# Kernel optimization log

Hardware: AMD Instinct MI355X
Metric: run time of the kernel (lower is better)

Reference implementation:

```python
import jax, jax.numpy as jnp
import numpy as np

B, H, S, DK = 2, 16, 2048, 64


def setup_inputs() -> dict:
    key = jax.random.key(0)
    kq, kk, kv, km = jax.random.split(key, 4)
    query = jax.random.normal(kq, (B, H, S, DK), dtype=jnp.float32)
    key_t = jax.random.normal(kk, (B, H, S, DK), dtype=jnp.float32)
    value = jax.random.normal(kv, (B, H, S, DK), dtype=jnp.float32)
    mask = jax.random.randint(km, (1, 1, S, S), 0, 2, dtype=jnp.int32)
    return {"query": query, "key": key_t, "value": value, "mask": mask}


def reference(query, key, value, mask):
    # scores: [B, H, Sq, Sk]
    d_k = query.shape[-1]
    scale = 1.0 / jnp.sqrt(jnp.asarray(d_k, dtype=query.dtype))
    scores = jnp.einsum("bhqd,bhkd->bhqk", query, key) * scale
    scores = jnp.where(mask == 0, jnp.asarray(-1e9, dtype=scores.dtype), scores)
    attention_weights = jax.nn.softmax(scores, axis=-1)
    # dropout is identity in eval mode (deterministic reference)
    output = jnp.einsum("bhqk,bhkd->bhqd", attention_weights, value)
    return output, attention_weights
```

## Files before the change

kernel.cpp:

```cpp
#include <hip/hip_runtime.h>
#include <hip/hip_bf16.h>


namespace {

constexpr int Bc = 2, Hc = 16, Sc = 2048, Dc = 64;
constexpr int QT = 64;
constexpr int KT = 64;
constexpr int NKV = Sc / KT;
constexpr int NQB = Sc / QT;
constexpr int NBH = Bc * Hc;
constexpr float SCALE2 = 0.125f * 1.44269504088896340736f;

constexpr int PS_OFF = 0;
constexpr int KS_OFF = 8192;
constexpr int VS_OFF = 24576;

constexpr size_t BITS_BYTES = (size_t)Sc * Sc / 8;
constexpr size_t IMG_BYTES  = (size_t)NBH * NKV * 8192;
constexpr size_t KIMG_OFF   = BITS_BYTES;
constexpr size_t VIMG_OFF   = BITS_BYTES + IMG_BYTES;
constexpr size_t WS_FULL    = BITS_BYTES + 2 * IMG_BYTES;

using short8 = __attribute__((ext_vector_type(8))) short;
using f32x4  = __attribute__((ext_vector_type(4))) float;
using u32x4  = __attribute__((ext_vector_type(4))) unsigned;

__device__ __forceinline__ int swz(int row, int bytecol) {
    return row * 128 + (bytecol ^ ((row & 7) << 4));
}

__device__ __forceinline__ unsigned cvtpk(float a, float b) {
    unsigned r;
    asm("v_cvt_pk_bf16_f32 %0, %1, %2" : "=v"(r) : "v"(a), "v"(b));
    return r;
}

__device__ __forceinline__ f32x4 mfma16(short8 a, short8 b, f32x4 c) {
    return __builtin_amdgcn_mfma_f32_16x16x32_bf16(a, b, c, 0, 0, 0);
}
__device__ __forceinline__ short8 ldlds(const char* lds, int off, int row,
                                        int bytecol) {
    return *reinterpret_cast<const short8*>(lds + off + swz(row, bytecol));
}

__device__ __forceinline__ void bar_lgkm() {
    __builtin_amdgcn_sched_barrier(0);
    asm volatile("s_waitcnt lgkmcnt(0)" ::: "memory");
    __builtin_amdgcn_s_barrier();
    __builtin_amdgcn_sched_barrier(0);
}
__device__ __forceinline__ void fence_lgkm() {
    __builtin_amdgcn_sched_barrier(0);
    asm volatile("s_waitcnt lgkmcnt(0)" ::: "memory");
    __builtin_amdgcn_sched_barrier(0);
}

__device__ __forceinline__ void ldk_g(const float* __restrict__ src, int tid,
                                      float4 reg[4]) {
    #pragma unroll
    for (int i = 0; i < 4; ++i) {
        int ch = tid + 256 * i;
        int r = ch >> 4, d0 = (ch & 15) << 2;
        reg[i] = *reinterpret_cast<const float4*>(src + (size_t)r * Dc + d0);
    }
}
__device__ __forceinline__ void stk_g(char* dst, int off, int tid,
                                      const float4 reg[4]) {
    #pragma unroll
    for (int i = 0; i < 4; ++i) {
        int ch = tid + 256 * i;
        int r = ch >> 4, d0 = (ch & 15) << 2;
        uint2 pk; pk.x = cvtpk(reg[i].x, reg[i].y);
        pk.y = cvtpk(reg[i].z, reg[i].w);
        *reinterpret_cast<uint2*>(dst + off + swz(r, d0 * 2)) = pk;
    }
}
__device__ __forceinline__ void ldv_g(const float* __restrict__ src, int tid,
                                      float4 reg[4]) {
    int d0 = (tid & 15) << 2, c0 = (tid >> 4) << 2;
    #pragma unroll
    for (int i = 0; i < 4; ++i)
        reg[i] = *reinterpret_cast<const float4*>(src + (size_t)(c0 + i) * Dc + d0);
}
__device__ __forceinline__ void stv_g(char* dst, int off, int tid,
                                      const float4 reg[4]) {
    int d0 = (tid & 15) << 2, c0 = (tid >> 4) << 2;
    uint2 pk;
    pk.x = cvtpk(reg[0].x, reg[1].x); pk.y = cvtpk(reg[2].x, reg[3].x);
    *reinterpret_cast<uint2*>(dst + off + swz(d0 + 0, c0 * 2)) = pk;
    pk.x = cvtpk(reg[0].y, reg[1].y); pk.y = cvtpk(reg[2].y, reg[3].y);
    *reinterpret_cast<uint2*>(dst + off + swz(d0 + 1, c0 * 2)) = pk;
    pk.x = cvtpk(reg[0].z, reg[1].z); pk.y = cvtpk(reg[2].z, reg[3].z);
    *reinterpret_cast<uint2*>(dst + off + swz(d0 + 2, c0 * 2)) = pk;
    pk.x = cvtpk(reg[0].w, reg[1].w); pk.y = cvtpk(reg[2].w, reg[3].w);
    *reinterpret_cast<uint2*>(dst + off + swz(d0 + 3, c0 * 2)) = pk;
}

__global__ __launch_bounds__(256) void pack_mask(
    const int* __restrict__ Mg, unsigned long long* __restrict__ bits)
{
    int tg = blockIdx.x * 256 + threadIdx.x;
    int v = Mg[tg];
    unsigned long long b = __ballot(v != 0);
    if ((threadIdx.x & 63) == 0) bits[tg >> 6] = b;
}

__global__ __launch_bounds__(256) void pack_kv(
    const float* __restrict__ Kg, const float* __restrict__ Vg,
    char* __restrict__ kimg, char* __restrict__ vimg)
{
    const int b = blockIdx.x;
    const int bh = b >> 5, kv = b & 31;
    const int t = threadIdx.x;
    const size_t off = (size_t)bh * Sc * Dc + (size_t)kv * KT * Dc;
    float4 kreg[4];
    ldk_g(Kg + off, t, kreg);
    stk_g(kimg + (size_t)b * 8192, 0, t, kreg);
    float4 vreg[4];
    ldv_g(Vg + off, t, vreg);
    stv_g(vimg + (size_t)b * 8192, 0, t, vreg);
}

template <int MODE>
__global__ __launch_bounds__(256, 4)
void attn_main(const float* __restrict__ Qg, const float* __restrict__ Kg,
               const float* __restrict__ Vg, const int* __restrict__ Mg,
               const unsigned* __restrict__ mbits,
               const char* __restrict__ kimg, const char* __restrict__ vimg,
               float* __restrict__ Og, float* __restrict__ Wg)
{
    constexpr bool USE_BITS = (MODE >= 1);
    __shared__ char lds_s[40960];
    char* lds = lds_s;

    const int bid = blockIdx.x;
    const int xcd = bid & 7, idx = bid >> 3;
    const int bh  = xcd * 4 + (idx & 3);
    const int qb  = idx >> 2;

    const int t    = threadIdx.x;
    const int lane = t & 63;
    const int w    = t >> 6;
    const int l15  = lane & 15, hi4 = lane >> 4;
    const int qw   = 16 * w;

    const size_t bh_off = (size_t)bh * Sc * Dc;
    const float* Qb = Qg + bh_off + (size_t)qb * QT * Dc;
    const float* Kb = Kg + bh_off;
    const float* Vb = Vg + bh_off;
    float* Ob = Og + bh_off + (size_t)qb * QT * Dc;
    float* Wb = Wg + (size_t)bh * Sc * Sc + (size_t)qb * QT * Sc;

    const int ql0 = qw + l15;
    const int qg0 = qb * QT + ql0;

    {
        float4 qreg[4];
        ldk_g(Qb, t, qreg);
        #pragma unroll
        for (int i = 0; i < 4; ++i) {
            int ch = t + 256 * i;
            int r = ch >> 4, d0 = (ch & 15) << 2;
            uint2 pk;
            pk.x = cvtpk(qreg[i].x * SCALE2, qreg[i].y * SCALE2);
            pk.y = cvtpk(qreg[i].z * SCALE2, qreg[i].w * SCALE2);
            *reinterpret_cast<uint2*>(lds + PS_OFF + swz(r, d0 * 2)) = pk;
        }
    }
    if constexpr (MODE == 2) {
        const char* src = kimg + (size_t)(bh * 32) * 8192 + t * 16;
        *reinterpret_cast<u32x4*>(lds + KS_OFF + t * 16) =
            *reinterpret_cast<const u32x4*>(src);
        *reinterpret_cast<u32x4*>(lds + KS_OFF + t * 16 + 4096) =
            *reinterpret_cast<const u32x4*>(src + 4096);
    } else {
        float4 kreg[4];
        ldk_g(Kb, t, kreg);
        stk_g(lds, KS_OFF, t, kreg);
    }
    bar_lgkm();

    short8 qf[2];
    #pragma unroll
    for (int kk = 0; kk < 2; ++kk)
        qf[kk] = ldlds(lds, PS_OFF, qw + l15, kk * 64 + hi4 * 16);

    float lsum = 0.f;

    for (int kv = 0; kv < NKV; ++kv) {
        const int nx = (kv + 1) & (NKV - 1);
        const int cko = KS_OFF + (kv & 1) * 8192;
        float4 sreg[4], vreg[4];
        u32x4 s0, s1, v0, v1;
        if constexpr (MODE == 2) {
            const char* src = kimg + (size_t)(bh * 32 + nx) * 8192 + t * 16;
            s0 = *reinterpret_cast<const u32x4*>(src);
            s1 = *reinterpret_cast<const u32x4*>(src + 4096);
            if (kv == NKV - 1) {
                const char* vs = vimg + (size_t)(bh * 32) * 8192 + t * 16;
                v0 = *reinterpret_cast<const u32x4*>(vs);
                v1 = *reinterpret_cast<const u32x4*>(vs + 4096);
            }
        } else {
            ldk_g(Kb + (size_t)nx * KT * Dc, t, sreg);
            if (kv == NKV - 1) ldv_g(Vb, t, vreg);
        }

        uint2 mb0;
        if (USE_BITS)
            mb0 = *reinterpret_cast<const uint2*>(mbits + (size_t)qg0 * 64 + kv * 2);

        f32x4 sc[4];
        #pragma unroll
        for (int ct = 0; ct < 4; ++ct) sc[ct] = f32x4{0.f, 0.f, 0.f, 0.f};
        #pragma unroll
        for (int kk = 0; kk < 2; ++kk) {
            int bc = kk * 64 + hi4 * 16;
            #pragma unroll
            for (int ct = 0; ct < 4; ++ct) {
                short8 kf = ldlds(lds, cko, ct * 16 + l15, bc);
                sc[ct] = mfma16(kf, qf[kk], sc[ct]);
            }
        }

        {
            float acc = 0.f;
            #pragma unroll
            for (int ct = 0; ct < 4; ++ct) {
                unsigned word = (ct >= 2) ? mb0.y : mb0.x;
                #pragma unroll
                for (int r = 0; r < 4; ++r) {
                    bool keep;
                    if (USE_BITS)
                        keep = (word >> ((ct & 1) * 16 + hi4 * 4 + r)) & 1;
                    else
                        keep = Mg[(size_t)qg0 * Sc + kv * KT + ct * 16 + hi4 * 4 + r] != 0;
                    acc += keep ? exp2f(sc[ct][r]) : 0.0f;
                }
            }
            lsum += acc;
        }

        if constexpr (MODE == 2) {
            char* d = lds + KS_OFF + (nx & 1) * 8192 + t * 16;
            *reinterpret_cast<u32x4*>(d) = s0;
            *reinterpret_cast<u32x4*>(d + 4096) = s1;
            if (kv == NKV - 1) {
                char* dv = lds + VS_OFF + t * 16;
                *reinterpret_cast<u32x4*>(dv) = v0;
                *reinterpret_cast<u32x4*>(dv + 4096) = v1;
            }
        } else {
            stk_g(lds, KS_OFF + (nx & 1) * 8192, t, sreg);
            if (kv == NKV - 1) stv_g(lds, VS_OFF, t, vreg);
        }
        bar_lgkm();
    }

    float rls;
    {
        float s = lsum;
        s += __shfl_xor(s, 16);
        s += __shfl_xor(s, 32);
        rls = 1.0f / s;
    }

    f32x4 oa[4];
    #pragma unroll
    for (int dt = 0; dt < 4; ++dt) oa[dt] = f32x4{0.f, 0.f, 0.f, 0.f};

    for (int kv = 0; kv < NKV; ++kv) {
        const bool pf = (kv + 1) < NKV;
        const int cko = KS_OFF + (kv & 1) * 8192;
        const int cvo = VS_OFF + (kv & 1) * 8192;
        float4 sreg[4], vreg[4];
        u32x4 s0, s1, s2, s3;
        if (pf) {
            if constexpr (MODE == 2) {
                const int ht = t & 127;
                const char* src = (t < 128)
                    ? kimg + (size_t)(bh * 32 + kv + 1) * 8192 + ht * 16
                    : vimg + (size_t)(bh * 32 + kv + 1) * 8192 + ht * 16;
                s0 = *reinterpret_cast<const u32x4*>(src);
                s1 = *reinterpret_cast<const u32x4*>(src + 2048);
                s2 = *reinterpret_cast<const u32x4*>(src + 4096);
                s3 = *reinterpret_cast<const u32x4*>(src + 6144);
            } else {
                ldk_g(Kb + (size_t)(kv + 1) * KT * Dc, t, sreg);
                ldv_g(Vb + (size_t)(kv + 1) * KT * Dc, t, vreg);
            }
        }

        uint2 mb0;
        if (USE_BITS)
            mb0 = *reinterpret_cast<const uint2*>(mbits + (size_t)qg0 * 64 + kv * 2);

        f32x4 sc[4];
        #pragma unroll
        for (int ct = 0; ct < 4; ++ct) sc[ct] = f32x4{0.f, 0.f, 0.f, 0.f};
        #pragma unroll
        for (int kk = 0; kk < 2; ++kk) {
            int bc = kk * 64 + hi4 * 16;
            #pragma unroll
            for (int ct = 0; ct < 4; ++ct) {
                short8 kf = ldlds(lds, cko, ct * 16 + l15, bc);
                sc[ct] = mfma16(kf, qf[kk], sc[ct]);
            }
        }

        #pragma unroll
        for (int ct = 0; ct < 4; ++ct) {
            unsigned word = (ct >= 2) ? mb0.y : mb0.x;
            float p[4];
            #pragma unroll
            for (int r = 0; r < 4; ++r) {
                bool keep;
                if (USE_BITS)
                    keep = (word >> ((ct & 1) * 16 + hi4 * 4 + r)) & 1;
                else
                    keep = Mg[(size_t)qg0 * Sc + kv * KT + ct * 16 + hi4 * 4 + r] != 0;
                p[r] = keep ? exp2f(sc[ct][r]) * rls : 0.0f;
            }
            uint2 pp; pp.x = cvtpk(p[0], p[1]); pp.y = cvtpk(p[2], p[3]);
            *reinterpret_cast<uint2*>(
                lds + PS_OFF + swz(ql0, ct * 32 + hi4 * 8)) = pp;
        }
        fence_lgkm();

        #pragma unroll
        for (int kk = 0; kk < 2; ++kk) {
            int bc = kk * 64 + hi4 * 16;
            short8 a0 = ldlds(lds, PS_OFF, qw + l15, bc);
            #pragma unroll
            for (int dt = 0; dt < 4; ++dt) {
                short8 b = ldlds(lds, cvo, dt * 16 + l15, bc);
                oa[dt] = mfma16(a0, b, oa[dt]);
            }
        }

        #pragma unroll
        for (int j = 0; j < 4; ++j) {
            int row = qw + j * 4 + hi4;
            uint2 pw = *reinterpret_cast<const uint2*>(
                lds + PS_OFF + swz(row, l15 * 8));
            f32x4 wv;
            wv[0] = __uint_as_float(pw.x << 16);
            wv[1] = __uint_as_float(pw.x & 0xffff0000u);
            wv[2] = __uint_as_float(pw.y << 16);
            wv[3] = __uint_as_float(pw.y & 0xffff0000u);
            __builtin_nontemporal_store(
                wv, reinterpret_cast<f32x4*>(
                    Wb + (size_t)row * Sc + kv * KT + l15 * 4));
        }

        if (pf) {
            if constexpr (MODE == 2) {
                const int ht = t & 127;
                char* d = (t < 128)
                    ? lds + KS_OFF + ((kv + 1) & 1) * 8192 + ht * 16
                    : lds + VS_OFF + ((kv + 1) & 1) * 8192 + ht * 16;
                *reinterpret_cast<u32x4*>(d) = s0;
                *reinterpret_cast<u32x4*>(d + 2048) = s1;
                *reinterpret_cast<u32x4*>(d + 4096) = s2;
                *reinterpret_cast<u32x4*>(d + 6144) = s3;
            } else {
                stk_g(lds, KS_OFF + ((kv + 1) & 1) * 8192, t, sreg);
                stv_g(lds, VS_OFF + ((kv + 1) & 1) * 8192, t, vreg);
            }
        }
        bar_lgkm();
    }

    #pragma unroll
    for (int dt = 0; dt < 4; ++dt)
        #pragma unroll
        for (int r = 0; r < 4; ++r) {
            int ql = qw + hi4 * 4 + r;
            __builtin_nontemporal_store(
                oa[dt][r], Ob + (size_t)ql * Dc + dt * 16 + l15);
        }
}

}

extern "C" void kernel_launch(void* const* d_in, const int* in_sizes, int n_in,
                              void* d_out, int out_size, void* d_ws, size_t ws_size,
                              hipStream_t stream) {
    const float* Qg = (const float*)d_in[0];
    const float* Kg = (const float*)d_in[1];
    const float* Vg = (const float*)d_in[2];
    const int*   Mg = (const int*)d_in[3];
    float* out_o = (float*)d_out;
    float* out_w = out_o + (size_t)Bc * Hc * Sc * Dc;

    char* ws = (char*)d_ws;
    dim3 grid(NQB * NBH), blk(256);

    if (d_ws != nullptr && ws_size >= WS_FULL) {
        unsigned long long* bits = (unsigned long long*)ws;
        char* kimg = ws + KIMG_OFF;
        char* vimg = ws + VIMG_OFF;
        pack_mask<<<(Sc * Sc) / 256, 256, 0, stream>>>(Mg, bits);
        pack_kv<<<NBH * NKV, 256, 0, stream>>>(Kg, Vg, kimg, vimg);
        attn_main<2><<<grid, blk, 0, stream>>>(
            Qg, Kg, Vg, Mg, (const unsigned*)bits, kimg, vimg, out_o, out_w);
    } else if (d_ws != nullptr && ws_size >= BITS_BYTES) {
        pack_mask<<<(Sc * Sc) / 256, 256, 0, stream>>>(
            Mg, (unsigned long long*)ws);
        attn_main<1><<<grid, blk, 0, stream>>>(
            Qg, Kg, Vg, Mg, (const unsigned*)ws, nullptr, nullptr, out_o, out_w);
    } else {
        attn_main<0><<<grid, blk, 0, stream>>>(
            Qg, Kg, Vg, Mg, nullptr, nullptr, nullptr, out_o, out_w);
    }
}
```

Baseline: 194.3 us.

## Process two K tiles per iteration in the row-sum pass with four LDS buffers

The first pass, which computes the softmax denominators, now handles two K tiles per loop iteration. It prefetches the next pair into a four-slot LDS ring, which halves the number of barriers and loads the mask bits as one 16-byte read. The first K and V tiles for the second pass are reloaded afterwards with an extra barrier. This uses more LDS (the ring spans 8192..40960 and overlaps VS_OFF, which is only safe because V is written after the loop) and more registers, which may reduce occupancy.

```diff
diff --git a/kernel.cpp b/kernel.cpp
--- a/kernel.cpp
+++ b/kernel.cpp
@@ -169,15 +169,20 @@
         }
     }
     if constexpr (MODE == 2) {
-        const char* src = kimg + (size_t)(bh * 32) * 8192 + t * 16;
-        *reinterpret_cast<u32x4*>(lds + KS_OFF + t * 16) =
-            *reinterpret_cast<const u32x4*>(src);
-        *reinterpret_cast<u32x4*>(lds + KS_OFF + t * 16 + 4096) =
-            *reinterpret_cast<const u32x4*>(src + 4096);
+        #pragma unroll
+        for (int j = 0; j < 2; ++j) {
+            const char* src = kimg + (size_t)(bh * 32 + j) * 8192 + t * 16;
+            char* d = lds + 8192 + j * 8192 + t * 16;
+            *reinterpret_cast<u32x4*>(d) = *reinterpret_cast<const u32x4*>(src);
+            *reinterpret_cast<u32x4*>(d + 4096) =
+                *reinterpret_cast<const u32x4*>(src + 4096);
+        }
     } else {
         float4 kreg[4];
         ldk_g(Kb, t, kreg);
-        stk_g(lds, KS_OFF, t, kreg);
+        stk_g(lds, 8192, t, kreg);
+        ldk_g(Kb + (size_t)KT * Dc, t, kreg);
+        stk_g(lds, 16384, t, kreg);
     }
     bar_lgkm();
 
@@ -188,75 +193,103 @@
 
     float lsum = 0.f;
 
-    for (int kv = 0; kv < NKV; ++kv) {
-        const int nx = (kv + 1) & (NKV - 1);
-        const int cko = KS_OFF + (kv & 1) * 8192;
-        float4 sreg[4], vreg[4];
-        u32x4 s0, s1, v0, v1;
-        if constexpr (MODE == 2) {
-            const char* src = kimg + (size_t)(bh * 32 + nx) * 8192 + t * 16;
-            s0 = *reinterpret_cast<const u32x4*>(src);
-            s1 = *reinterpret_cast<const u32x4*>(src + 4096);
-            if (kv == NKV - 1) {
-                const char* vs = vimg + (size_t)(bh * 32) * 8192 + t * 16;
-                v0 = *reinterpret_cast<const u32x4*>(vs);
-                v1 = *reinterpret_cast<const u32x4*>(vs + 4096);
-            }
-        } else {
-            ldk_g(Kb + (size_t)nx * KT * Dc, t, sreg);
-            if (kv == NKV - 1) ldv_g(Vb, t, vreg);
-        }
-
-        uint2 mb0;
+    for (int kv = 0; kv < NKV; kv += 2) {
+        const bool pf = (kv + 2) < NKV;
+        u32x4 a0, a1, b0, b1;
+        float4 sregA[4], sregB[4];
+        if (pf) {
+            if constexpr (MODE == 2) {
+                const char* sa = kimg + (size_t)(bh * 32 + kv + 2) * 8192 + t * 16;
+                a0 = *reinterpret_cast<const u32x4*>(sa);
+                a1 = *reinterpret_cast<const u32x4*>(sa + 4096);
+                const char* sb = kimg + (size_t)(bh * 32 + kv + 3) * 8192 + t * 16;
+                b0 = *reinterpret_cast<const u32x4*>(sb);
+                b1 = *reinterpret_cast<const u32x4*>(sb + 4096);
+            } else {
+                ldk_g(Kb + (size_t)(kv + 2) * KT * Dc, t, sregA);
+                ldk_g(Kb + (size_t)(kv + 3) * KT * Dc, t, sregB);
+            }
+        }
+
+        uint4 mb4;
         if (USE_BITS)
-            mb0 = *reinterpret_cast<const uint2*>(mbits + (size_t)qg0 * 64 + kv * 2);
-
-        f32x4 sc[4];
-        #pragma unroll
-        for (int ct = 0; ct < 4; ++ct) sc[ct] = f32x4{0.f, 0.f, 0.f, 0.f};
-        #pragma unroll
-        for (int kk = 0; kk < 2; ++kk) {
-            int bc = kk * 64 + hi4 * 16;
+            mb4 = *reinterpret_cast<const uint4*>(
+                mbits + (size_t)qg0 * 64 + kv * 2);
+
+        #pragma unroll
+        for (int j = 0; j < 2; ++j) {
+            const int cko = 8192 + ((kv + j) & 3) * 8192;
+            f32x4 sc[4];
+            #pragma unroll
+            for (int ct = 0; ct < 4; ++ct) sc[ct] = f32x4{0.f, 0.f, 0.f, 0.f};
+            #pragma unroll
+            for (int kk = 0; kk < 2; ++kk) {
+                int bc = kk * 64 + hi4 * 16;
+                #pragma unroll
+                for (int ct = 0; ct < 4; ++ct) {
+                    short8 kf = ldlds(lds, cko, ct * 16 + l15, bc);
+                    sc[ct] = mfma16(kf, qf[kk], sc[ct]);
+                }
+            }
+            unsigned wlo = 0, whi = 0;
+            if (USE_BITS) {
+                wlo = j ? mb4.z : mb4.x;
+                whi = j ? mb4.w : mb4.y;
+            }
+            float acc = 0.f;
             #pragma unroll
             for (int ct = 0; ct < 4; ++ct) {
-                short8 kf = ldlds(lds, cko, ct * 16 + l15, bc);
-                sc[ct] = mfma16(kf, qf[kk], sc[ct]);
-            }
-        }
-
-        {
-            float acc = 0.f;
-            #pragma unroll
-            for (int ct = 0; ct < 4; ++ct) {
-                unsigned word = (ct >= 2) ? mb0.y : mb0.x;
+                unsigned word = (ct >= 2) ? whi : wlo;
                 #pragma unroll
                 for (int r = 0; r < 4; ++r) {
                     bool keep;
                     if (USE_BITS)
                         keep = (word >> ((ct & 1) * 16 + hi4 * 4 + r)) & 1;
                     else
-                        keep = Mg[(size_t)qg0 * Sc + kv * KT + ct * 16 + hi4 * 4 + r] != 0;
+                        keep = Mg[(size_t)qg0 * Sc + (kv + j) * KT
+                                  + ct * 16 + hi4 * 4 + r] != 0;
                     acc += keep ? exp2f(sc[ct][r]) : 0.0f;
                 }
             }
             lsum += acc;
         }
 
-        if constexpr (MODE == 2) {
-            char* d = lds + KS_OFF + (nx & 1) * 8192 + t * 16;
-            *reinterpret_cast<u32x4*>(d) = s0;
-            *reinterpret_cast<u32x4*>(d + 4096) = s1;
-            if (kv == NKV - 1) {
-                char* dv = lds + VS_OFF + t * 16;
-                *reinterpret_cast<u32x4*>(dv) = v0;
-                *reinterpret_cast<u32x4*>(dv + 4096) = v1;
-            }
-        } else {
-            stk_g(lds, KS_OFF + (nx & 1) * 8192, t, sreg);
-            if (kv == NKV - 1) stv_g(lds, VS_OFF, t, vreg);
+        if (pf) {
+            if constexpr (MODE == 2) {
+                char* da = lds + 8192 + ((kv + 2) & 3) * 8192 + t * 16;
+                *reinterpret_cast<u32x4*>(da) = a0;
+                *reinterpret_cast<u32x4*>(da + 4096) = a1;
+                char* db = lds + 8192 + ((kv + 3) & 3) * 8192 + t * 16;
+                *reinterpret_cast<u32x4*>(db) = b0;
+                *reinterpret_cast<u32x4*>(db + 4096) = b1;
+            } else {
+                stk_g(lds, 8192 + ((kv + 2) & 3) * 8192, t, sregA);
+                stk_g(lds, 8192 + ((kv + 3) & 3) * 8192, t, sregB);
+            }
         }
         bar_lgkm();
     }
+
+    if constexpr (MODE == 2) {
+        const char* sk = kimg + (size_t)(bh * 32) * 8192 + t * 16;
+        *reinterpret_cast<u32x4*>(lds + KS_OFF + t * 16) =
+            *reinterpret_cast<const u32x4*>(sk);
+        *reinterpret_cast<u32x4*>(lds + KS_OFF + t * 16 + 4096) =
+            *reinterpret_cast<const u32x4*>(sk + 4096);
+        const char* sv = vimg + (size_t)(bh * 32) * 8192 + t * 16;
+        *reinterpret_cast<u32x4*>(lds + VS_OFF + t * 16) =
+            *reinterpret_cast<const u32x4*>(sv);
+        *reinterpret_cast<u32x4*>(lds + VS_OFF + t * 16 + 4096) =
+            *reinterpret_cast<const u32x4*>(sv + 4096);
+    } else {
+        float4 kreg[4];
+        ldk_g(Kb, t, kreg);
+        stk_g(lds, KS_OFF, t, kreg);
+        float4 vreg[4];
+        ldv_g(Vb, t, vreg);
+        stv_g(lds, VS_OFF, t, vreg);
+    }
+    bar_lgkm();
 
     float rls;
     {
```

New measurement: 197.6 us. No clear change (+1.7%).

## Double-buffer P tile in LDS and write attention weights every two KV blocks

Applied to the files above, without the earlier changes.

The P staging area in LDS grows to hold two consecutive 64-column KV tiles. The attention-weight writeback now runs every other iteration, with each lane storing 32 contiguous bytes (two 16-byte nontemporal stores) per row instead of 16. The aim is to make the large fp32 weight writes wider and more contiguous. In exchange, LDS use rises to 48KB and launch bounds drop to 3 blocks per CU, which may lower occupancy.

```diff
diff --git a/kernel.cpp b/kernel.cpp
--- a/kernel.cpp
+++ b/kernel.cpp
@@ -13,8 +13,8 @@
 constexpr float SCALE2 = 0.125f * 1.44269504088896340736f;
 
 constexpr int PS_OFF = 0;
-constexpr int KS_OFF = 8192;
-constexpr int VS_OFF = 24576;
+constexpr int KS_OFF = 16384;
+constexpr int VS_OFF = 32768;
 
 constexpr size_t BITS_BYTES = (size_t)Sc * Sc / 8;
 constexpr size_t IMG_BYTES  = (size_t)NBH * NKV * 8192;
@@ -28,6 +28,9 @@
 
 __device__ __forceinline__ int swz(int row, int bytecol) {
     return row * 128 + (bytecol ^ ((row & 7) << 4));
+}
+__device__ __forceinline__ int pswz(int row, int bytecol) {
+    return row * 256 + (bytecol ^ ((row & 7) << 4));
 }
 
 __device__ __forceinline__ unsigned cvtpk(float a, float b) {
@@ -123,7 +126,7 @@
 }
 
 template <int MODE>
-__global__ __launch_bounds__(256, 4)
+__global__ __launch_bounds__(256, 3)
 void attn_main(const float* __restrict__ Qg, const float* __restrict__ Kg,
                const float* __restrict__ Vg, const int* __restrict__ Mg,
                const unsigned* __restrict__ mbits,
@@ -131,7 +134,7 @@
                float* __restrict__ Og, float* __restrict__ Wg)
 {
     constexpr bool USE_BITS = (MODE >= 1);
-    __shared__ char lds_s[40960];
+    __shared__ char lds_s[49152];
     char* lds = lds_s;
 
     const int bid = blockIdx.x;
@@ -165,7 +168,7 @@
             uint2 pk;
             pk.x = cvtpk(qreg[i].x * SCALE2, qreg[i].y * SCALE2);
             pk.y = cvtpk(qreg[i].z * SCALE2, qreg[i].w * SCALE2);
-            *reinterpret_cast<uint2*>(lds + PS_OFF + swz(r, d0 * 2)) = pk;
+            *reinterpret_cast<uint2*>(lds + PS_OFF + pswz(r, d0 * 2)) = pk;
         }
     }
     if constexpr (MODE == 2) {
@@ -184,7 +187,8 @@
     short8 qf[2];
     #pragma unroll
     for (int kk = 0; kk < 2; ++kk)
-        qf[kk] = ldlds(lds, PS_OFF, qw + l15, kk * 64 + hi4 * 16);
+        qf[kk] = *reinterpret_cast<const short8*>(
+            lds + PS_OFF + pswz(qw + l15, kk * 64 + hi4 * 16));
 
     float lsum = 0.f;
 
@@ -274,6 +278,7 @@
         const bool pf = (kv + 1) < NKV;
         const int cko = KS_OFF + (kv & 1) * 8192;
         const int cvo = VS_OFF + (kv & 1) * 8192;
+        const int psj = (kv & 1) * 128;
         float4 sreg[4], vreg[4];
         u32x4 s0, s1, s2, s3;
         if (pf) {
@@ -324,14 +329,15 @@
             }
             uint2 pp; pp.x = cvtpk(p[0], p[1]); pp.y = cvtpk(p[2], p[3]);
             *reinterpret_cast<uint2*>(
-                lds + PS_OFF + swz(ql0, ct * 32 + hi4 * 8)) = pp;
+                lds + PS_OFF + pswz(ql0, psj + ct * 32 + hi4 * 8)) = pp;
         }
         fence_lgkm();
 
         #pragma unroll
         for (int kk = 0; kk < 2; ++kk) {
             int bc = kk * 64 + hi4 * 16;
-            short8 a0 = ldlds(lds, PS_OFF, qw + l15, bc);
+            short8 a0 = *reinterpret_cast<const short8*>(
+                lds + PS_OFF + pswz(qw + l15, psj + bc));
             #pragma unroll
             for (int dt = 0; dt < 4; ++dt) {
                 short8 b = ldlds(lds, cvo, dt * 16 + l15, bc);
@@ -339,19 +345,25 @@
             }
         }
 
-        #pragma unroll
-        for (int j = 0; j < 4; ++j) {
-            int row = qw + j * 4 + hi4;
-            uint2 pw = *reinterpret_cast<const uint2*>(
-                lds + PS_OFF + swz(row, l15 * 8));
-            f32x4 wv;
-            wv[0] = __uint_as_float(pw.x << 16);
-            wv[1] = __uint_as_float(pw.x & 0xffff0000u);
-            wv[2] = __uint_as_float(pw.y << 16);
-            wv[3] = __uint_as_float(pw.y & 0xffff0000u);
-            __builtin_nontemporal_store(
-                wv, reinterpret_cast<f32x4*>(
-                    Wb + (size_t)row * Sc + kv * KT + l15 * 4));
+        if (kv & 1) {
+            #pragma unroll
+            for (int j = 0; j < 4; ++j) {
+                int row = qw + j * 4 + hi4;
+                u32x4 pw = *reinterpret_cast<const u32x4*>(
+                    lds + PS_OFF + pswz(row, l15 * 16));
+                f32x4 w0, w1;
+                w0[0] = __uint_as_float(pw[0] << 16);
+                w0[1] = __uint_as_float(pw[0] & 0xffff0000u);
+                w0[2] = __uint_as_float(pw[1] << 16);
+                w0[3] = __uint_as_float(pw[1] & 0xffff0000u);
+                w1[0] = __uint_as_float(pw[2] << 16);
+                w1[1] = __uint_as_float(pw[2] & 0xffff0000u);
+                w1[2] = __uint_as_float(pw[3] << 16);
+                w1[3] = __uint_as_float(pw[3] & 0xffff0000u);
+                float* wr = Wb + (size_t)row * Sc + (kv - 1) * KT + l15 * 8;
+                __builtin_nontemporal_store(w0, reinterpret_cast<f32x4*>(wr));
+                __builtin_nontemporal_store(w1, reinterpret_cast<f32x4*>(wr + 4));
+            }
         }
 
         if (pf) {
```

Measured after the change: 259.9 us. +33.8%, slower.
